# Kernel tuning notes

Measured on AMD Instinct MI355X. Metric: run time of the kernel, lower is better.

## Reference

```python
import jax, jax.numpy as jnp
import numpy as np

N, L, C, NHEAD = 4, 2048, 1024, 8
D = C // NHEAD
EPS_ATTN = 1e-6
EPS_LN = 1e-5


def _w(key, shape, scale=0.02):
    return jax.random.normal(key, shape, dtype=jnp.float32) * scale


def setup_inputs() -> dict:
    key = jax.random.key(0)
    ks = jax.random.split(key, 32)
    inp = {
        'depth_feat': jax.random.normal(ks[0], (N, L, C), dtype=jnp.float32),
        'context_feat': jax.random.normal(ks[1], (N, L, C), dtype=jnp.float32),
        'depth_pos': jax.random.normal(ks[2], (N, L, C), dtype=jnp.float32),
        # encoder params (weights stored [in, out]; y = x @ W)
        'e_wq': _w(ks[3], (C, C)), 'e_wk': _w(ks[4], (C, C)), 'e_wv': _w(ks[5], (C, C)),
        'e_wm': _w(ks[6], (C, C)),
        'e_w1': _w(ks[7], (C, 2 * C)), 'e_w2': _w(ks[8], (2 * C, C)),
        'e_g1': jnp.ones((C,), jnp.float32), 'e_b1': jnp.zeros((C,), jnp.float32),
        'e_g2': jnp.ones((C,), jnp.float32), 'e_b2': jnp.zeros((C,), jnp.float32),
        # decoder params
        'd_wq0': _w(ks[9], (C, C)), 'd_wk0': _w(ks[10], (C, C)), 'd_wv0': _w(ks[11], (C, C)),
        'd_wm0': _w(ks[12], (C, C)),
        'd_wq1': _w(ks[13], (C, C)), 'd_wk1': _w(ks[14], (C, C)), 'd_wv1': _w(ks[15], (C, C)),
        'd_wm1': _w(ks[16], (C, C)),
        'd_w1': _w(ks[17], (C, 2 * C)), 'd_w2': _w(ks[18], (2 * C, C)),
        'd_g0': jnp.ones((C,), jnp.float32), 'd_b0': jnp.zeros((C,), jnp.float32),
        'd_g1': jnp.ones((C,), jnp.float32), 'd_b1': jnp.zeros((C,), jnp.float32),
        'd_g2': jnp.ones((C,), jnp.float32), 'd_b2': jnp.zeros((C,), jnp.float32),
    }
    return inp


def layernorm(x, g, b):
    m = jnp.mean(x, axis=-1, keepdims=True)
    v = jnp.mean(jnp.square(x - m), axis=-1, keepdims=True)
    return (x - m) * jax.lax.rsqrt(v + EPS_LN) * g + b


def linear_attention(q, k, v):
    # q,k,v: [N, L, H, D]; elu+1 feature map, O(L) kernelized attention
    Q = jax.nn.elu(q) + 1.0
    K = jax.nn.elu(k) + 1.0
    vlen = v.shape[1]
    v = v / vlen
    KV = jnp.einsum('nshd,nshv->nhdv', K, v)                    # [N,H,D,D]
    Z = 1.0 / (jnp.einsum('nlhd,nhd->nlh', Q, K.sum(axis=1)) + EPS_ATTN)
    out = jnp.einsum('nlhd,nhdv,nlh->nlhv', Q, KV, Z) * vlen    # [N,L,H,D]
    return out


def heads(x):
    n, l, c = x.shape
    return x.reshape(n, l, NHEAD, D)


def encoder_layer(x, wq, wk, wv, wm, w1, w2, g1, b1, g2, b2):
    n, l, c = x.shape
    msg = linear_attention(heads(x @ wq), heads(x @ wk), heads(x @ wv))
    msg = msg.reshape(n, l, c) @ wm
    x = x + layernorm(msg, g1, b1)
    x = x + layernorm(jax.nn.relu(x @ w1) @ w2, g2, b2)
    return x


def decoder_layer(x, src, wq0, wk0, wv0, wm0, wq1, wk1, wv1, wm1, w1, w2, g0, b0, g1, b1, g2, b2):
    n, l, c = x.shape
    msg = linear_attention(heads(x @ wq0), heads(x @ wk0), heads(x @ wv0))
    msg = msg.reshape(n, l, c) @ wm0
    x = x + layernorm(msg, g0, b0)
    msg = linear_attention(heads(x @ wq1), heads(src @ wk1), heads(src @ wv1))
    msg = msg.reshape(n, l, c) @ wm1
    x = x + layernorm(msg, g1, b1)
    x = x + layernorm(jax.nn.relu(x @ w1) @ w2, g2, b2)
    return x


def reference(depth_feat, context_feat, depth_pos,
              e_wq, e_wk, e_wv, e_wm, e_w1, e_w2, e_g1, e_b1, e_g2, e_b2,
              d_wq0, d_wk0, d_wv0, d_wm0, d_wq1, d_wk1, d_wv1, d_wm1,
              d_w1, d_w2, d_g0, d_b0, d_g1, d_b1, d_g2, d_b2):
    ctx = context_feat + depth_pos
    ctx = encoder_layer(ctx, e_wq, e_wk, e_wv, e_wm, e_w1, e_w2, e_g1, e_b1, e_g2, e_b2)
    out = decoder_layer(depth_feat, ctx,
                        d_wq0, d_wk0, d_wv0, d_wm0,
                        d_wq1, d_wk1, d_wv1, d_wm1,
                        d_w1, d_w2, d_g0, d_b0, d_g1, d_b1, d_g2, d_b2)
    return out
```

## Files before the change

kernel.cpp:

```cpp
#include <hip/hip_runtime.h>
#include <cstdint>

#define N_B 4
#define L_S 2048
#define C_F 1024
#define H_N 8
#define D_H 128
#define M_T (N_B * L_S)

typedef __bf16 bf16;
typedef __bf16 bf16x4 __attribute__((ext_vector_type(4)));
typedef __bf16 bf16x8 __attribute__((ext_vector_type(8)));
typedef float f32x4 __attribute__((ext_vector_type(4)));

typedef __attribute__((address_space(1))) void gvoid_t;
typedef __attribute__((address_space(3))) void lvoid_t;

__device__ __forceinline__ void lds_cp16(void* lds, const void* g) {
    __builtin_amdgcn_global_load_lds((gvoid_t*)g, (lvoid_t*)lds, 16, 0, 0);
}

__device__ __forceinline__ float elup1(float x) {
    return x > 0.0f ? x + 1.0f : __expf(x);
}

__device__ __forceinline__ void load4f(const void* base, size_t e0, int isbf, float* o) {
    if (isbf) {
        bf16x4 v = *(const bf16x4*)((const bf16*)base + e0);
        o[0] = (float)v[0]; o[1] = (float)v[1]; o[2] = (float)v[2]; o[3] = (float)v[3];
    } else {
        float4 v = *(const float4*)((const float*)base + e0);
        o[0] = v.x; o[1] = v.y; o[2] = v.z; o[3] = v.w;
    }
}

__device__ __forceinline__ int xcd_swz(int wgid, int nwg) {
    return (wgid & 7) * (nwg >> 3) + (wgid >> 3);
}

__global__ void detect_dtype(const unsigned int* g1, int* flag) {
    if (threadIdx.x == 0 && blockIdx.x == 0)
        *flag = (g1[0] == 0x3F803F80u) ? 1 : 0;
}

__global__ __launch_bounds__(256) void transpose_any(
        const void* __restrict__ src, bf16* __restrict__ dst,
        int R, int Cc, const int* __restrict__ flagp) {
    const int isbf = *flagp;
    __shared__ bf16 tile[32][33];
    const int bx = blockIdx.x * 32;
    const int by = blockIdx.y * 32;
    const int tx = threadIdx.x & 31;
    const int ty = threadIdx.x >> 5;
#pragma unroll
    for (int i = 0; i < 32; i += 8) {
        size_t ix = (size_t)(by + ty + i) * Cc + bx + tx;
        float v = isbf ? (float)((const bf16*)src)[ix] : ((const float*)src)[ix];
        tile[ty + i][tx] = (bf16)v;
    }
    __syncthreads();
#pragma unroll
    for (int i = 0; i < 32; i += 8)
        dst[(size_t)(bx + ty + i) * R + by + tx] = tile[tx][ty + i];
}

struct TAll {
    const void* src[16];
    unsigned int dstoff[16];
    int R[16];
    int C[16];
    int tile0[17];
};

__global__ __launch_bounds__(256) void transpose_all(
        TAll p, bf16* __restrict__ twall, const int* __restrict__ flagp) {
    const int isbf = *flagp;
    int gid = blockIdx.x;
    int w = 0;
    while (gid >= p.tile0[w + 1]) ++w;
    const int local = gid - p.tile0[w];
    const int R = p.R[w], Cc = p.C[w];
    const int tilesx = Cc >> 5;
    const int bx = (local % tilesx) * 32;
    const int by = (local / tilesx) * 32;
    const void* src = p.src[w];
    bf16* dst = twall + p.dstoff[w];
    __shared__ bf16 tile[32][33];
    const int tx = threadIdx.x & 31;
    const int ty = threadIdx.x >> 5;
#pragma unroll
    for (int i = 0; i < 32; i += 8) {
        size_t ix = (size_t)(by + ty + i) * Cc + bx + tx;
        float v = isbf ? (float)((const bf16*)src)[ix] : ((const float*)src)[ix];
        tile[ty + i][tx] = (bf16)v;
    }
    __syncthreads();
#pragma unroll
    for (int i = 0; i < 32; i += 8)
        dst[(size_t)(bx + ty + i) * R + by + tx] = tile[tx][ty + i];
}

template <int ACT>
__global__ __launch_bounds__(256, 2) void gemm_bt(
        const bf16* __restrict__ A, const bf16* __restrict__ Bt,
        bf16* __restrict__ C, int M, int N, int K) {
    __shared__ bf16 sA[128 * 64];
    __shared__ bf16 sB[128 * 64];
    const int t = threadIdx.x;
    const int lane = t & 63;
    const int w = t >> 6;
    const int wm = (w >> 1) * 64, wn = (w & 1) * 64;
    const int lr = lane & 15, lq = lane >> 4;
    const int gx = gridDim.x;
    const int nwg = gx * gridDim.y;
    const int wgid = xcd_swz(blockIdx.y * gx + blockIdx.x, nwg);
    const int m0 = (wgid / gx) * 128, n0 = (wgid % gx) * 128;

    f32x4 acc[4][4] = {};

    for (int kt = 0; kt < K; kt += 64) {
        const bf16* Ag = A + (size_t)m0 * K + kt;
        const bf16* Bg = Bt + (size_t)n0 * K + kt;
#pragma unroll
        for (int i = 0; i < 4; ++i) {
            int ci = t + i * 256;
            int r = ci >> 3, c8 = (ci & 7) * 8;
            lds_cp16(&sA[ci * 8], Ag + (size_t)r * K + c8);
        }
#pragma unroll
        for (int i = 0; i < 4; ++i) {
            int ci = t + i * 256;
            int r = ci >> 3, c8 = (ci & 7) * 8;
            lds_cp16(&sB[ci * 8], Bg + (size_t)r * K + c8);
        }
        __syncthreads();
#pragma unroll
        for (int kk = 0; kk < 64; kk += 32) {
            bf16x8 af[4], bfr[4];
#pragma unroll
            for (int mi = 0; mi < 4; ++mi)
                af[mi] = *(const bf16x8*)&sA[(wm + mi * 16 + lr) * 64 + kk + lq * 8];
#pragma unroll
            for (int ni = 0; ni < 4; ++ni)
                bfr[ni] = *(const bf16x8*)&sB[(wn + ni * 16 + lr) * 64 + kk + lq * 8];
#pragma unroll
            for (int mi = 0; mi < 4; ++mi)
#pragma unroll
                for (int ni = 0; ni < 4; ++ni)
                    acc[mi][ni] = __builtin_amdgcn_mfma_f32_16x16x32_bf16(
                        af[mi], bfr[ni], acc[mi][ni], 0, 0, 0);
        }
        __syncthreads();
    }
#pragma unroll
    for (int mi = 0; mi < 4; ++mi)
#pragma unroll
        for (int ni = 0; ni < 4; ++ni)
#pragma unroll
            for (int r = 0; r < 4; ++r) {
                int row = m0 + wm + mi * 16 + lq * 4 + r;
                int col = n0 + wn + ni * 16 + lr;
                float v = acc[mi][ni][r];
                if (ACT == 1) v = fmaxf(v, 0.0f);
                if (ACT == 2) v = v > 0.0f ? v + 1.0f : __expf(v);
                C[(size_t)row * N + col] = (bf16)v;
            }
}

#define STAGE_T(sarr, Gbase, ldstride, Tt)                                    \
    {                                                                         \
        const int sl_ = (Tt) & 3;                                             \
        _Pragma("unroll")                                                     \
        for (int i_ = 0; i_ < 2; ++i_) {                                      \
            int ci_ = t + i_ * 512;                                           \
            int r_ = ci_ >> 2, c8_ = (ci_ & 3) * 8;                           \
            lds_cp16(&sarr[sl_ * 8192 + ci_ * 8],                             \
                     (Gbase) + (size_t)r_ * (ldstride) + ((Tt) << 5) +        \
                         (c8_ ^ ((r_ & 3) << 3)));                            \
        }                                                                     \
    }

template <int ACT>
__global__ __launch_bounds__(512, 2) void gemm256(
        const bf16* __restrict__ A, const bf16* __restrict__ Bt,
        bf16* __restrict__ C, int M, int N, int K, int actsplit) {
    __shared__ bf16 sA[4 * 256 * 32];
    __shared__ bf16 sB[4 * 256 * 32];
    const int t = threadIdx.x;
    const int lane = t & 63;
    const int w = t >> 6;
    const int wr = w >> 2, wc = w & 3;
    const int lr = lane & 15, lq = lane >> 4;
    const int gx = gridDim.x;
    const int nwg = gx * gridDim.y;
    const int wgid = xcd_swz(blockIdx.y * gx + blockIdx.x, nwg);
    const int m0 = (wgid / gx) * 256, n0 = (wgid % gx) * 256;
    const int nt = K >> 5;

    const bf16* Ab = A + (size_t)m0 * K;
    const bf16* Bb = Bt + (size_t)n0 * K;

    f32x4 acc[8][4] = {};

    STAGE_T(sA, Ab, K, 0); STAGE_T(sB, Bb, K, 0);
    STAGE_T(sA, Ab, K, 1); STAGE_T(sB, Bb, K, 1);
    asm volatile("s_waitcnt vmcnt(4)" ::: "memory");
    __builtin_amdgcn_s_barrier();

    for (int T = 0; T < nt; ++T) {
        const bf16* sAs = &sA[(T & 3) * 8192];
        const bf16* sBs = &sB[(T & 3) * 8192];
        bf16x8 af[4], bfr[4], ag[4];
#pragma unroll
        for (int mi = 0; mi < 4; ++mi) {
            int row = wr * 128 + mi * 16 + lr;
            af[mi] = *(const bf16x8*)&sAs[row * 32 + ((lq * 8) ^ ((row & 3) << 3))];
        }
#pragma unroll
        for (int ni = 0; ni < 4; ++ni) {
            int row = wc * 64 + ni * 16 + lr;
            bfr[ni] = *(const bf16x8*)&sBs[row * 32 + ((lq * 8) ^ ((row & 3) << 3))];
        }
        if (T + 2 < nt) STAGE_T(sA, Ab, K, T + 2);
        __builtin_amdgcn_s_barrier();
        __builtin_amdgcn_s_setprio(1);
#pragma unroll
        for (int mi = 0; mi < 4; ++mi)
#pragma unroll
            for (int ni = 0; ni < 4; ++ni)
                acc[mi][ni] = __builtin_amdgcn_mfma_f32_16x16x32_bf16(
                    af[mi], bfr[ni], acc[mi][ni], 0, 0, 0);
        __builtin_amdgcn_s_setprio(0);
        __builtin_amdgcn_s_barrier();
#pragma unroll
        for (int mi = 0; mi < 4; ++mi) {
            int row = wr * 128 + (mi + 4) * 16 + lr;
            ag[mi] = *(const bf16x8*)&sAs[row * 32 + ((lq * 8) ^ ((row & 3) << 3))];
        }
        if (T + 2 < nt) STAGE_T(sB, Bb, K, T + 2);
        __builtin_amdgcn_s_barrier();
        __builtin_amdgcn_s_setprio(1);
#pragma unroll
        for (int mi = 0; mi < 4; ++mi)
#pragma unroll
            for (int ni = 0; ni < 4; ++ni)
                acc[mi + 4][ni] = __builtin_amdgcn_mfma_f32_16x16x32_bf16(
                    ag[mi], bfr[ni], acc[mi + 4][ni], 0, 0, 0);
        __builtin_amdgcn_s_setprio(0);
        if (T + 1 < nt) {
            if (T + 2 < nt) asm volatile("s_waitcnt vmcnt(4)" ::: "memory");
            else            asm volatile("s_waitcnt vmcnt(0)" ::: "memory");
        }
        __builtin_amdgcn_s_barrier();
    }
#pragma unroll
    for (int mi = 0; mi < 8; ++mi)
#pragma unroll
        for (int ni = 0; ni < 4; ++ni)
#pragma unroll
            for (int r = 0; r < 4; ++r) {
                int row = m0 + wr * 128 + mi * 16 + lq * 4 + r;
                int col = n0 + wc * 64 + ni * 16 + lr;
                float v = acc[mi][ni][r];
                if (ACT == 1) v = fmaxf(v, 0.0f);
                if (ACT == 3 && row < actsplit) v = v > 0.0f ? v + 1.0f : __expf(v);
                C[(size_t)row * N + col] = (bf16)v;
            }
}

__global__ __launch_bounds__(256, 2) void attn_kv_mfma(
        const bf16* __restrict__ ktg, const bf16* __restrict__ vtg,
        bf16* __restrict__ KVp, float* __restrict__ KSp) {
    const int nh = blockIdx.x;
    const int chunk = blockIdx.y;
    const int n = nh >> 3, h = nh & 7;
    const int t = threadIdx.x;
    const int lane = t & 63;
    const int w = t >> 6;
    const int wm = (w >> 1) * 64, wn = (w & 1) * 64;
    const int lr = lane & 15, lq = lane >> 4;
    __shared__ bf16 sA[128 * 64];
    __shared__ bf16 sB[128 * 64];
    const size_t base = (size_t)(h * D_H) * M_T + (size_t)n * L_S + chunk * 128;

    f32x4 acc[4][4] = {};
    float ks = 0.0f;
    const int dh = t >> 1, half = (t & 1) * 32;

    for (int kt = 0; kt < 128; kt += 64) {
        const bf16* Ag = vtg + base + kt;
        const bf16* Bg = ktg + base + kt;
#pragma unroll
        for (int i = 0; i < 4; ++i) {
            int ci = t + i * 256;
            int r = ci >> 3, c8 = (ci & 7) * 8;
            lds_cp16(&sA[ci * 8], Ag + (size_t)r * M_T + c8);
        }
#pragma unroll
        for (int i = 0; i < 4; ++i) {
            int ci = t + i * 256;
            int r = ci >> 3, c8 = (ci & 7) * 8;
            lds_cp16(&sB[ci * 8], Bg + (size_t)r * M_T + c8);
        }
        __syncthreads();
#pragma unroll
        for (int j = 0; j < 4; ++j) {
            bf16x8 v = *(const bf16x8*)&sB[dh * 64 + half + j * 8];
#pragma unroll
            for (int m = 0; m < 8; ++m) ks += (float)v[m];
        }
#pragma unroll
        for (int kk = 0; kk < 64; kk += 32) {
            bf16x8 af[4], bfr[4];
#pragma unroll
            for (int mi = 0; mi < 4; ++mi)
                af[mi] = *(const bf16x8*)&sA[(wm + mi * 16 + lr) * 64 + kk + lq * 8];
#pragma unroll
            for (int ni = 0; ni < 4; ++ni)
                bfr[ni] = *(const bf16x8*)&sB[(wn + ni * 16 + lr) * 64 + kk + lq * 8];
#pragma unroll
            for (int mi = 0; mi < 4; ++mi)
#pragma unroll
                for (int ni = 0; ni < 4; ++ni)
                    acc[mi][ni] = __builtin_amdgcn_mfma_f32_16x16x32_bf16(
                        af[mi], bfr[ni], acc[mi][ni], 0, 0, 0);
        }
        __syncthreads();
    }
    float ko = __shfl_xor(ks, 1);
    if (!(t & 1)) KSp[(nh * 16 + chunk) * D_H + dh] = ks + ko;

    bf16* out = KVp + ((size_t)(nh * 16 + chunk)) * (D_H * D_H);
#pragma unroll
    for (int mi = 0; mi < 4; ++mi)
#pragma unroll
        for (int ni = 0; ni < 4; ++ni)
#pragma unroll
            for (int r = 0; r < 4; ++r) {
                int row = wm + mi * 16 + lq * 4 + r;
                int col = wn + ni * 16 + lr;
                out[(size_t)row * D_H + col] = (bf16)acc[mi][ni][r];
            }
}

__global__ __launch_bounds__(256) void attn_reduce_t(
        const bf16* __restrict__ KVp, const float* __restrict__ KSp,
        bf16* __restrict__ KVt, float* __restrict__ Ksum) {
    const int nh = blockIdx.x;
    const int es = blockIdx.y;
    const int t = threadIdx.x;
    const size_t base = (size_t)nh * 16 * (D_H * D_H) + es * 4096 + t * 16;
    float fa[16] = {};
    for (int c = 0; c < 16; ++c) {
        const bf16* p = KVp + base + (size_t)c * (D_H * D_H);
        bf16x8 a = *(const bf16x8*)p;
        bf16x8 b = *(const bf16x8*)(p + 8);
#pragma unroll
        for (int m = 0; m < 8; ++m) { fa[m] += (float)a[m]; fa[8 + m] += (float)b[m]; }
    }
    bf16* o = KVt + (size_t)nh * (D_H * D_H) + es * 4096 + t * 16;
    bf16x8 oa, ob;
#pragma unroll
    for (int m = 0; m < 8; ++m) { oa[m] = (bf16)fa[m]; ob[m] = (bf16)fa[8 + m]; }
    *(bf16x8*)o = oa;
    *(bf16x8*)(o + 8) = ob;
    if (es == 0 && t < 128) {
        float s = 0.0f;
#pragma unroll
        for (int c = 0; c < 16; ++c) s += KSp[(nh * 16 + c) * D_H + t];
        Ksum[nh * D_H + t] = s;
    }
}

__global__ __launch_bounds__(256, 2) void attn_out_mfma(
        const bf16* __restrict__ qb, const bf16* __restrict__ KVt,
        const float* __restrict__ Ksum, bf16* __restrict__ ab) {
    const int nh = blockIdx.x, tile = blockIdx.y;
    const int n = nh >> 3, h = nh & 7;
    const int t = threadIdx.x;
    const int lane = t & 63;
    const int w = t >> 6;
    const int wm = (w >> 1) * 64, wn = (w & 1) * 64;
    const int lr = lane & 15, lq = lane >> 4;
    __shared__ bf16 sA[128 * 64];
    __shared__ bf16 sB[128 * 64];
    __shared__ float sKs[128];
    __shared__ float sZp[128][2];
    __shared__ float sZ[128];
    if (t < 128) sKs[t] = Ksum[nh * D_H + t];

    f32x4 acc[4][4] = {};
    float zacc = 0.0f;
    const int zrow = t >> 1, zoff = (t & 1) * 32;
    const size_t qbase = ((size_t)(n * L_S + tile * 128)) * C_F + h * D_H;

    for (int kt = 0; kt < 128; kt += 64) {
        __syncthreads();
#pragma unroll
        for (int i = 0; i < 4; ++i) {
            int ci = t + i * 256;
            int r = ci >> 3, c8 = (ci & 7) * 8;
            lds_cp16(&sA[ci * 8], qb + qbase + (size_t)r * C_F + kt + c8);
            lds_cp16(&sB[ci * 8], KVt + (size_t)nh * (D_H * D_H) + (size_t)r * D_H + kt + c8);
        }
        __syncthreads();
#pragma unroll 8
        for (int j = 0; j < 32; ++j)
            zacc += (float)sA[zrow * 64 + zoff + j] * sKs[kt + zoff + j];
#pragma unroll
        for (int kk = 0; kk < 64; kk += 32) {
            bf16x8 af[4], bfr[4];
#pragma unroll
            for (int mi = 0; mi < 4; ++mi)
                af[mi] = *(const bf16x8*)&sA[(wm + mi * 16 + lr) * 64 + kk + lq * 8];
#pragma unroll
            for (int ni = 0; ni < 4; ++ni)
                bfr[ni] = *(const bf16x8*)&sB[(wn + ni * 16 + lr) * 64 + kk + lq * 8];
#pragma unroll
            for (int mi = 0; mi < 4; ++mi)
#pragma unroll
                for (int ni = 0; ni < 4; ++ni)
                    acc[mi][ni] = __builtin_amdgcn_mfma_f32_16x16x32_bf16(
                        af[mi], bfr[ni], acc[mi][ni], 0, 0, 0);
        }
    }
    sZp[zrow][t & 1] = zacc;
    __syncthreads();
    if (t < 128) sZ[t] = 1.0f / (sZp[t][0] + sZp[t][1] + 1e-6f);
    __syncthreads();
#pragma unroll
    for (int mi = 0; mi < 4; ++mi)
#pragma unroll
        for (int ni = 0; ni < 4; ++ni)
#pragma unroll
            for (int r = 0; r < 4; ++r) {
                int row = wm + mi * 16 + lq * 4 + r;
                int col = wn + ni * 16 + lr;
                ab[qbase + (size_t)row * C_F + col] = (bf16)(acc[mi][ni][r] * sZ[row]);
            }
}

template <int F32OUT>
__global__ __launch_bounds__(256) void ln_res(
        const bf16* __restrict__ msg, const void* __restrict__ g,
        const void* __restrict__ bb, const int* __restrict__ flagp,
        const bf16* __restrict__ xin, void* __restrict__ xout) {
    const int isbf = *flagp;
    const int row = blockIdx.x * 4 + (threadIdx.x >> 6);
    const int lane = threadIdx.x & 63;
    const size_t base = (size_t)row * C_F;
    float m[16];
#pragma unroll
    for (int k = 0; k < 4; ++k) {
        bf16x4 v = *(const bf16x4*)(msg + base + k * 256 + lane * 4);
        m[k * 4 + 0] = (float)v[0]; m[k * 4 + 1] = (float)v[1];
        m[k * 4 + 2] = (float)v[2]; m[k * 4 + 3] = (float)v[3];
    }
    float s1 = 0.0f, s2 = 0.0f;
#pragma unroll
    for (int q = 0; q < 16; ++q) { s1 += m[q]; s2 += m[q] * m[q]; }
#pragma unroll
    for (int off = 32; off > 0; off >>= 1) {
        s1 += __shfl_down(s1, off);
        s2 += __shfl_down(s2, off);
    }
    s1 = __shfl(s1, 0);
    s2 = __shfl(s2, 0);
    const float mean = s1 / C_F;
    const float rs = rsqrtf(s2 / C_F - mean * mean + 1e-5f);
#pragma unroll
    for (int k = 0; k < 4; ++k) {
        const size_t cix = k * 256 + lane * 4;
        float ga[4], ba[4];
        load4f(g, cix, isbf, ga);
        load4f(bb, cix, isbf, ba);
        bf16x4 x4 = *(const bf16x4*)(xin + base + cix);
        if (F32OUT) {
            float4 of;
            of.x = (float)x4[0] + (m[k * 4 + 0] - mean) * rs * ga[0] + ba[0];
            of.y = (float)x4[1] + (m[k * 4 + 1] - mean) * rs * ga[1] + ba[1];
            of.z = (float)x4[2] + (m[k * 4 + 2] - mean) * rs * ga[2] + ba[2];
            of.w = (float)x4[3] + (m[k * 4 + 3] - mean) * rs * ga[3] + ba[3];
            *(float4*)((float*)xout + base + cix) = of;
        } else {
            bf16x4 ob;
            ob[0] = (bf16)((float)x4[0] + (m[k * 4 + 0] - mean) * rs * ga[0] + ba[0]);
            ob[1] = (bf16)((float)x4[1] + (m[k * 4 + 1] - mean) * rs * ga[1] + ba[1]);
            ob[2] = (bf16)((float)x4[2] + (m[k * 4 + 2] - mean) * rs * ga[2] + ba[2]);
            ob[3] = (bf16)((float)x4[3] + (m[k * 4 + 3] - mean) * rs * ga[3] + ba[3]);
            *(bf16x4*)((bf16*)xout + base + cix) = ob;
        }
    }
}

__global__ __launch_bounds__(256) void init_ctx_kernel(
        const void* __restrict__ a, const void* __restrict__ b,
        const int* __restrict__ flagp, bf16* __restrict__ xb) {
    const int isbf = *flagp;
    const size_t i = ((size_t)blockIdx.x * 256 + threadIdx.x) * 4;
    float av[4], bv[4];
    load4f(a, i, isbf, av);
    load4f(b, i, isbf, bv);
    bf16x4 o;
#pragma unroll
    for (int q = 0; q < 4; ++q) o[q] = (bf16)(av[q] + bv[q]);
    *(bf16x4*)(xb + i) = o;
}

__global__ __launch_bounds__(256) void conv_copy_kernel(
        const void* __restrict__ a, const int* __restrict__ flagp,
        bf16* __restrict__ xb) {
    const int isbf = *flagp;
    const size_t i = ((size_t)blockIdx.x * 256 + threadIdx.x) * 4;
    float av[4];
    load4f(a, i, isbf, av);
    bf16x4 o;
#pragma unroll
    for (int q = 0; q < 4; ++q) o[q] = (bf16)av[q];
    *(bf16x4*)(xb + i) = o;
}

extern "C" void kernel_launch(void* const* d_in, const int* in_sizes, int n_in,
                              void* d_out, int out_size, void* d_ws, size_t ws_size,
                              hipStream_t stream) {
    const size_t MB = 1u << 20;
    uint8_t* W = (uint8_t*)d_ws;
    bf16* xb    = (bf16*)(W + 0);
    bf16* ctxb  = (bf16*)(W + 16 * MB);
    bf16* qb    = (bf16*)(W + 32 * MB);
    bf16* kb    = (bf16*)(W + 48 * MB);
    bf16* vb    = (bf16*)(W + 64 * MB);
    bf16* hb    = kb;
    bf16* S     = (bf16*)(W + 80 * MB);
    bf16* TW    = (bf16*)(W + 96 * MB);
    bf16* KVp   = S;
    float* KSp  = (float*)(W + 100 * MB);
    bf16* KVt   = (bf16*)(W + 101 * MB);
    float* Ksum = (float*)(W + 102 * MB);
    int*   flag = (int*)(W + 102 * MB + 64 * 1024);
    bf16* TWall = (bf16*)(W + 104 * MB);
    const bool batched = (ws_size >= 145 * MB);

    detect_dtype<<<1, 64, 0, stream>>>((const unsigned int*)d_in[9], flag);

    const int widx[16] = {3,4,5,6,7,8,13,14,15,16,17,18,19,20,21,22};
    const int wR[16]   = {1024,1024,1024,1024,1024,2048,1024,1024,1024,1024,
                          1024,1024,1024,1024,1024,2048};
    const int wC[16]   = {1024,1024,1024,1024,2048,1024,1024,1024,1024,1024,
                          1024,1024,1024,1024,2048,1024};
    unsigned int off[16];
    {
        unsigned int acc = 0;
        for (int i = 0; i < 16; ++i) { off[i] = acc; acc += (unsigned int)wR[i] * wC[i]; }
    }
    if (batched) {
        TAll p;
        int tacc = 0;
        for (int i = 0; i < 16; ++i) {
            p.src[i] = d_in[widx[i]];
            p.dstoff[i] = off[i];
            p.R[i] = wR[i];
            p.C[i] = wC[i];
            p.tile0[i] = tacc;
            tacc += (wR[i] / 32) * (wC[i] / 32);
        }
        p.tile0[16] = tacc;
        transpose_all<<<tacc, 256, 0, stream>>>(p, TWall, flag);
    }
    auto SLOT = [&](int idx) {
        for (int i = 0; i < 16; ++i) if (widx[i] == idx) return i;
        return 0;
    };
    auto BT = [&](int idx) -> const bf16* {
        int s = SLOT(idx);
        if (batched) return TWall + off[s];
        dim3 g(wC[s] / 32, wR[s] / 32);
        transpose_any<<<g, 256, 0, stream>>>(d_in[idx], TW, wR[s], wC[s], flag);
        return TW;
    };
    auto TG = [&](int idx, const bf16* A, bf16* Cc, int Nn, int Kk, int act) {
        const bf16* Bt = BT(idx);
        dim3 g(Nn / 128, M_T / 128);
        if (act == 1)      gemm_bt<1><<<g, 256, 0, stream>>>(A, Bt, Cc, M_T, Nn, Kk);
        else if (act == 2) gemm_bt<2><<<g, 256, 0, stream>>>(A, Bt, Cc, M_T, Nn, Kk);
        else               gemm_bt<0><<<g, 256, 0, stream>>>(A, Bt, Cc, M_T, Nn, Kk);
    };
    auto KVF = [&](int kidx, int vidx, const bf16* X) {
        const bf16* Wt;
        if (batched) {
            Wt = TWall + off[SLOT(kidx)];
        } else {
            dim3 g(32, 32);
            transpose_any<<<g, 256, 0, stream>>>(d_in[kidx], TW, 1024, 1024, flag);
            transpose_any<<<g, 256, 0, stream>>>(d_in[vidx], TW + 1024 * 1024, 1024, 1024, flag);
            Wt = TW;
        }
        dim3 g(M_T / 256, (2 * C_F) / 256);
        gemm256<3><<<g, 512, 0, stream>>>(Wt, X, kb, 2 * C_F, M_T, C_F, C_F);
    };
    auto FFN1 = [&](int idx, const bf16* A) {
        const bf16* Bt = BT(idx);
        dim3 g((2 * C_F) / 256, M_T / 256);
        gemm256<1><<<g, 512, 0, stream>>>(A, Bt, hb, M_T, 2 * C_F, C_F, 0);
    };
    auto ATT = [&](const bf16* q, const bf16* k, const bf16* v, bf16* o) {
        attn_kv_mfma<<<dim3(32, 16), 256, 0, stream>>>(k, v, KVp, KSp);
        attn_reduce_t<<<dim3(32, 4), 256, 0, stream>>>(KVp, KSp, KVt, Ksum);
        attn_out_mfma<<<dim3(32, 16), 256, 0, stream>>>(q, KVt, Ksum, o);
    };
    auto LN = [&](const bf16* m, int gi, int bi, const bf16* xi, bf16* xo) {
        ln_res<0><<<M_T / 4, 256, 0, stream>>>(m, d_in[gi], d_in[bi], flag, xi, (void*)xo);
    };

    init_ctx_kernel<<<M_T * C_F / 1024, 256, 0, stream>>>(d_in[1], d_in[2], flag, xb);
    TG(3, xb, qb, C_F, C_F, 2);
    KVF(4, 5, xb);
    ATT(qb, kb, vb, S);
    TG(6, S, qb, C_F, C_F, 0);
    LN(qb, 9, 10, xb, xb);
    FFN1(7, xb);
    TG(8, hb, S, C_F, 2 * C_F, 0);
    LN(S, 11, 12, xb, ctxb);

    conv_copy_kernel<<<M_T * C_F / 1024, 256, 0, stream>>>(d_in[0], flag, xb);
    TG(13, xb, qb, C_F, C_F, 2);
    KVF(14, 15, xb);
    ATT(qb, kb, vb, S);
    TG(16, S, qb, C_F, C_F, 0);
    LN(qb, 23, 24, xb, xb);
    TG(17, xb, qb, C_F, C_F, 2);
    KVF(18, 19, ctxb);
    ATT(qb, kb, vb, S);
    TG(20, S, qb, C_F, C_F, 0);
    LN(qb, 25, 26, xb, xb);
    FFN1(21, xb);
    TG(22, hb, S, C_F, 2 * C_F, 0);
    ln_res<1><<<M_T / 4, 256, 0, stream>>>(S, d_in[27], d_in[28], flag, xb, d_out);
}
```

Before: 870.0 us.

## Double-buffer LDS tiles in gemm_bt and attention MFMA kernels

Converts the single-buffered LDS staging in gemm_bt, attn_kv_mfma and attn_out_mfma into a two-buffer ping-pong. The global-to-LDS copies for the next K tile are issued before the MFMA work on the current tile. The aim is to hide global load latency behind matrix math instead of stalling on every tile. This doubles LDS use per block to about 64KB, which may limit how many blocks fit per CU. The attention kernels run only two K iterations, so there is little to overlap there.

```diff
diff --git a/kernel.cpp b/kernel.cpp
--- a/kernel.cpp
+++ b/kernel.cpp
@@ -104,8 +104,8 @@
 __global__ __launch_bounds__(256, 2) void gemm_bt(
         const bf16* __restrict__ A, const bf16* __restrict__ Bt,
         bf16* __restrict__ C, int M, int N, int K) {
-    __shared__ bf16 sA[128 * 64];
-    __shared__ bf16 sB[128 * 64];
+    __shared__ bf16 sA[2][128 * 64];
+    __shared__ bf16 sB[2][128 * 64];
     const int t = threadIdx.x;
     const int lane = t & 63;
     const int w = t >> 6;
@@ -116,33 +116,42 @@
     const int wgid = xcd_swz(blockIdx.y * gx + blockIdx.x, nwg);
     const int m0 = (wgid / gx) * 128, n0 = (wgid % gx) * 128;
 
+    const bf16* Ab = A + (size_t)m0 * K;
+    const bf16* Bb = Bt + (size_t)n0 * K;
+
     f32x4 acc[4][4] = {};
 
-    for (int kt = 0; kt < K; kt += 64) {
-        const bf16* Ag = A + (size_t)m0 * K + kt;
-        const bf16* Bg = Bt + (size_t)n0 * K + kt;
-#pragma unroll
-        for (int i = 0; i < 4; ++i) {
-            int ci = t + i * 256;
-            int r = ci >> 3, c8 = (ci & 7) * 8;
-            lds_cp16(&sA[ci * 8], Ag + (size_t)r * K + c8);
-        }
-#pragma unroll
-        for (int i = 0; i < 4; ++i) {
-            int ci = t + i * 256;
-            int r = ci >> 3, c8 = (ci & 7) * 8;
-            lds_cp16(&sB[ci * 8], Bg + (size_t)r * K + c8);
-        }
-        __syncthreads();
+#define GSTAGE(buf, kt)                                                       \
+    {                                                                         \
+        _Pragma("unroll")                                                     \
+        for (int i_ = 0; i_ < 4; ++i_) {                                      \
+            int ci_ = t + i_ * 256;                                           \
+            int r_ = ci_ >> 3, c8_ = (ci_ & 7) * 8;                           \
+            lds_cp16(&sA[buf][ci_ * 8], Ab + (size_t)r_ * K + (kt) + c8_);    \
+        }                                                                     \
+        _Pragma("unroll")                                                     \
+        for (int i_ = 0; i_ < 4; ++i_) {                                      \
+            int ci_ = t + i_ * 256;                                           \
+            int r_ = ci_ >> 3, c8_ = (ci_ & 7) * 8;                           \
+            lds_cp16(&sB[buf][ci_ * 8], Bb + (size_t)r_ * K + (kt) + c8_);    \
+        }                                                                     \
+    }
+
+    GSTAGE(0, 0)
+    __syncthreads();
+
+    int b = 0;
+    for (int kt = 0; kt < K; kt += 64, b ^= 1) {
+        if (kt + 64 < K) GSTAGE(b ^ 1, kt + 64)
 #pragma unroll
         for (int kk = 0; kk < 64; kk += 32) {
             bf16x8 af[4], bfr[4];
 #pragma unroll
             for (int mi = 0; mi < 4; ++mi)
-                af[mi] = *(const bf16x8*)&sA[(wm + mi * 16 + lr) * 64 + kk + lq * 8];
+                af[mi] = *(const bf16x8*)&sA[b][(wm + mi * 16 + lr) * 64 + kk + lq * 8];
 #pragma unroll
             for (int ni = 0; ni < 4; ++ni)
-                bfr[ni] = *(const bf16x8*)&sB[(wn + ni * 16 + lr) * 64 + kk + lq * 8];
+                bfr[ni] = *(const bf16x8*)&sB[b][(wn + ni * 16 + lr) * 64 + kk + lq * 8];
 #pragma unroll
             for (int mi = 0; mi < 4; ++mi)
 #pragma unroll
@@ -152,6 +161,7 @@
         }
         __syncthreads();
     }
+#undef GSTAGE
 #pragma unroll
     for (int mi = 0; mi < 4; ++mi)
 #pragma unroll
@@ -279,33 +289,41 @@
     const int w = t >> 6;
     const int wm = (w >> 1) * 64, wn = (w & 1) * 64;
     const int lr = lane & 15, lq = lane >> 4;
-    __shared__ bf16 sA[128 * 64];
-    __shared__ bf16 sB[128 * 64];
+    __shared__ bf16 sA[2][128 * 64];
+    __shared__ bf16 sB[2][128 * 64];
     const size_t base = (size_t)(h * D_H) * M_T + (size_t)n * L_S + chunk * 128;
+    const bf16* Ag0 = vtg + base;
+    const bf16* Bg0 = ktg + base;
 
     f32x4 acc[4][4] = {};
     float ks = 0.0f;
     const int dh = t >> 1, half = (t & 1) * 32;
 
-    for (int kt = 0; kt < 128; kt += 64) {
-        const bf16* Ag = vtg + base + kt;
-        const bf16* Bg = ktg + base + kt;
-#pragma unroll
-        for (int i = 0; i < 4; ++i) {
-            int ci = t + i * 256;
-            int r = ci >> 3, c8 = (ci & 7) * 8;
-            lds_cp16(&sA[ci * 8], Ag + (size_t)r * M_T + c8);
-        }
-#pragma unroll
-        for (int i = 0; i < 4; ++i) {
-            int ci = t + i * 256;
-            int r = ci >> 3, c8 = (ci & 7) * 8;
-            lds_cp16(&sB[ci * 8], Bg + (size_t)r * M_T + c8);
-        }
-        __syncthreads();
+#define KVSTG(buf, kt)                                                        \
+    {                                                                         \
+        _Pragma("unroll")                                                     \
+        for (int i_ = 0; i_ < 4; ++i_) {                                      \
+            int ci_ = t + i_ * 256;                                           \
+            int r_ = ci_ >> 3, c8_ = (ci_ & 7) * 8;                           \
+            lds_cp16(&sA[buf][ci_ * 8], Ag0 + (size_t)r_ * M_T + (kt) + c8_); \
+        }                                                                     \
+        _Pragma("unroll")                                                     \
+        for (int i_ = 0; i_ < 4; ++i_) {                                      \
+            int ci_ = t + i_ * 256;                                           \
+            int r_ = ci_ >> 3, c8_ = (ci_ & 7) * 8;                           \
+            lds_cp16(&sB[buf][ci_ * 8], Bg0 + (size_t)r_ * M_T + (kt) + c8_); \
+        }                                                                     \
+    }
+
+    KVSTG(0, 0)
+    __syncthreads();
+
+    int b = 0;
+    for (int kt = 0; kt < 128; kt += 64, b ^= 1) {
+        if (kt + 64 < 128) KVSTG(b ^ 1, kt + 64)
 #pragma unroll
         for (int j = 0; j < 4; ++j) {
-            bf16x8 v = *(const bf16x8*)&sB[dh * 64 + half + j * 8];
+            bf16x8 v = *(const bf16x8*)&sB[b][dh * 64 + half + j * 8];
 #pragma unroll
             for (int m = 0; m < 8; ++m) ks += (float)v[m];
         }
@@ -314,10 +332,10 @@
             bf16x8 af[4], bfr[4];
 #pragma unroll
             for (int mi = 0; mi < 4; ++mi)
-                af[mi] = *(const bf16x8*)&sA[(wm + mi * 16 + lr) * 64 + kk + lq * 8];
+                af[mi] = *(const bf16x8*)&sA[b][(wm + mi * 16 + lr) * 64 + kk + lq * 8];
 #pragma unroll
             for (int ni = 0; ni < 4; ++ni)
-                bfr[ni] = *(const bf16x8*)&sB[(wn + ni * 16 + lr) * 64 + kk + lq * 8];
+                bfr[ni] = *(const bf16x8*)&sB[b][(wn + ni * 16 + lr) * 64 + kk + lq * 8];
 #pragma unroll
             for (int mi = 0; mi < 4; ++mi)
 #pragma unroll
@@ -327,6 +345,7 @@
         }
         __syncthreads();
     }
+#undef KVSTG
     float ko = __shfl_xor(ks, 1);
     if (!(t & 1)) KSp[(nh * 16 + chunk) * D_H + dh] = ks + ko;
 
@@ -382,8 +401,8 @@
     const int w = t >> 6;
     const int wm = (w >> 1) * 64, wn = (w & 1) * 64;
     const int lr = lane & 15, lq = lane >> 4;
-    __shared__ bf16 sA[128 * 64];
-    __shared__ bf16 sB[128 * 64];
+    __shared__ bf16 sA[2][128 * 64];
+    __shared__ bf16 sB[2][128 * 64];
     __shared__ float sKs[128];
     __shared__ float sZp[128][2];
     __shared__ float sZ[128];
@@ -393,29 +412,38 @@
     float zacc = 0.0f;
     const int zrow = t >> 1, zoff = (t & 1) * 32;
     const size_t qbase = ((size_t)(n * L_S + tile * 128)) * C_F + h * D_H;
-
-    for (int kt = 0; kt < 128; kt += 64) {
-        __syncthreads();
-#pragma unroll
-        for (int i = 0; i < 4; ++i) {
-            int ci = t + i * 256;
-            int r = ci >> 3, c8 = (ci & 7) * 8;
-            lds_cp16(&sA[ci * 8], qb + qbase + (size_t)r * C_F + kt + c8);
-            lds_cp16(&sB[ci * 8], KVt + (size_t)nh * (D_H * D_H) + (size_t)r * D_H + kt + c8);
-        }
-        __syncthreads();
+    const bf16* Bg0 = KVt + (size_t)nh * (D_H * D_H);
+
+#define OSTG(buf, kt)                                                         \
+    {                                                                         \
+        _Pragma("unroll")                                                     \
+        for (int i_ = 0; i_ < 4; ++i_) {                                      \
+            int ci_ = t + i_ * 256;                                           \
+            int r_ = ci_ >> 3, c8_ = (ci_ & 7) * 8;                           \
+            lds_cp16(&sA[buf][ci_ * 8],                                       \
+                     qb + qbase + (size_t)r_ * C_F + (kt) + c8_);             \
+            lds_cp16(&sB[buf][ci_ * 8], Bg0 + (size_t)r_ * D_H + (kt) + c8_); \
+        }                                                                     \
+    }
+
+    OSTG(0, 0)
+    __syncthreads();
+
+    int b = 0;
+    for (int kt = 0; kt < 128; kt += 64, b ^= 1) {
+        if (kt + 64 < 128) OSTG(b ^ 1, kt + 64)
 #pragma unroll 8
         for (int j = 0; j < 32; ++j)
-            zacc += (float)sA[zrow * 64 + zoff + j] * sKs[kt + zoff + j];
+            zacc += (float)sA[b][zrow * 64 + zoff + j] * sKs[kt + zoff + j];
 #pragma unroll
         for (int kk = 0; kk < 64; kk += 32) {
             bf16x8 af[4], bfr[4];
 #pragma unroll
             for (int mi = 0; mi < 4; ++mi)
-                af[mi] = *(const bf16x8*)&sA[(wm + mi * 16 + lr) * 64 + kk + lq * 8];
+                af[mi] = *(const bf16x8*)&sA[b][(wm + mi * 16 + lr) * 64 + kk + lq * 8];
 #pragma unroll
             for (int ni = 0; ni < 4; ++ni)
-                bfr[ni] = *(const bf16x8*)&sB[(wn + ni * 16 + lr) * 64 + kk + lq * 8];
+                bfr[ni] = *(const bf16x8*)&sB[b][(wn + ni * 16 + lr) * 64 + kk + lq * 8];
 #pragma unroll
             for (int mi = 0; mi < 4; ++mi)
 #pragma unroll
@@ -423,7 +451,9 @@
                     acc[mi][ni] = __builtin_amdgcn_mfma_f32_16x16x32_bf16(
                         af[mi], bfr[ni], acc[mi][ni], 0, 0, 0);
         }
-    }
+        __syncthreads();
+    }
+#undef OSTG
     sZp[zrow][t & 1] = zacc;
     __syncthreads();
     if (t < 128) sZ[t] = 1.0f / (sZp[t][0] + sZp[t][1] + 1e-6f);
```

Result: no change. 880.2 us (+1.2%).
